# Kernel tuning notes

Hardware: AMD Instinct MI355X
Metric: run time of the kernel (lower is better)

Reference implementation:

```python
import jax, jax.numpy as jnp
import numpy as np

PAD = 0
B, C, N, W = 64, 4, 32, 32   # batch, max cross, max nodes/sample, max words/bag
D = 512                       # d_model == d_word_vec
DK = 64                       # attention dim
VOCAB = 32000


def setup_inputs() -> dict:
    key = jax.random.key(0)
    ks = jax.random.split(key, 10)
    token_ids = jax.random.randint(ks[0], (B, C, N, W), 1, VOCAB)
    node_lengths = jax.random.randint(ks[1], (B * C * N,), 1, W + 1)
    node_sizes = jax.random.randint(ks[2], (B * C,), 1, N + 1)
    cross_lengths = jax.random.randint(ks[3], (B,), 1, C + 1)
    con_hidden = jax.random.normal(ks[4], (B, D), dtype=jnp.float32)
    emb = jax.random.normal(ks[5], (VOCAB, D), dtype=jnp.float32) * 0.02
    emb = emb.at[PAD].set(0.0)  # padding_idx row is zero
    W_pre = jax.random.normal(ks[6], (D, DK), dtype=jnp.float32) / np.sqrt(D).astype(np.float32)
    b_pre = jnp.zeros((DK,), dtype=jnp.float32)
    W_q = jax.random.normal(ks[7], (D, DK), dtype=jnp.float32) / np.sqrt(D).astype(np.float32)
    v = jax.random.normal(ks[8], (DK,), dtype=jnp.float32) / np.sqrt(DK).astype(np.float32)
    return dict(token_ids=token_ids, node_lengths=node_lengths,
                node_sizes=node_sizes, cross_lengths=cross_lengths,
                con_hidden=con_hidden, emb=emb, W_pre=W_pre, b_pre=b_pre,
                W_q=W_q, v=v)


def reference(token_ids, node_lengths, node_sizes, cross_lengths,
              con_hidden, emb, W_pre, b_pre, W_q, v):
    # hidden: flattened context vector per cross/sample  [B, D]
    hidden = con_hidden.reshape(con_hidden.shape[0], -1)

    # --- fused ragged gather-and-pad (replaces nested python loops) ---
    # bags[t] = zero-padded stack of word embeddings for bag t; T = B*C*N
    bags = emb[token_ids.reshape(-1, W)]                         # [T, W, D]
    word_mask = jnp.arange(W)[None, :] < node_lengths[:, None]   # [T, W]
    bags = bags * word_mask[:, :, None].astype(bags.dtype)

    # root per bag = hidden[cross_idx] repeated for every bag of that sample
    roots = jnp.repeat(hidden, C * N, axis=0)                    # [T, D]

    # --- ConcatAttention(roots, bags) ---
    pre = jnp.einsum('twd,dk->twk', bags, W_pre) + b_pre         # [T, W, DK]
    q = roots @ W_q                                              # [T, DK]
    energy = jnp.einsum('twk,k->tw', jnp.tanh(pre + q[:, None, :]), v)
    score = jax.nn.softmax(energy, axis=1)                       # [T, W]
    context = jnp.einsum('tw,twd->td', score, bags)              # [T, D]

    # --- repack contexts into [B, max_cross, max_node_size, D], PAD(=0)-filled ---
    out = context.reshape(B, C, N, D)
    node_mask = jnp.arange(N)[None, :] < node_sizes.reshape(B, C)[:, :, None]  # [B,C,N]
    cross_mask = jnp.arange(C)[None, :] < cross_lengths[:, None]               # [B,C]
    mask = node_mask & cross_mask[:, :, None]
    out = out * mask[..., None].astype(out.dtype)
    return out, hidden
```

## Files before the change

### kernel.cpp

```cpp
#include <hip/hip_runtime.h>
#include <hip/hip_bf16.h>

#define TB   8192
#define WW   32
#define DD   512
#define DKK  64
#define CCC  4

#define CONV_BLKS   2000

using bf16x8 = __attribute__((ext_vector_type(8))) short;
using f32x4  = __attribute__((ext_vector_type(4))) float;
using f32x2  = __attribute__((ext_vector_type(2))) float;

__device__ __forceinline__ unsigned short f2bf(float x) {
    union { float f; unsigned u; } u;
    u.f = x;
    unsigned r = u.u + 0x7fffu + ((u.u >> 16) & 1u);
    return (unsigned short)(r >> 16);
}

__device__ __forceinline__ bf16x8 make_frag(float4 x, float4 y) {
    union { bf16x8 v; unsigned short s[8]; } u;
    u.s[0] = f2bf(x.x); u.s[1] = f2bf(x.y); u.s[2] = f2bf(x.z); u.s[3] = f2bf(x.w);
    u.s[4] = f2bf(y.x); u.s[5] = f2bf(y.y); u.s[6] = f2bf(y.z); u.s[7] = f2bf(y.w);
    return u.v;
}

__device__ __forceinline__ uint2 pack_fp8x8(float4 a, float4 b) {
    int lo = 0, hi = 0;
    lo = __builtin_amdgcn_cvt_pk_fp8_f32(a.x, a.y, lo, false);
    lo = __builtin_amdgcn_cvt_pk_fp8_f32(a.z, a.w, lo, true);
    hi = __builtin_amdgcn_cvt_pk_fp8_f32(b.x, b.y, hi, false);
    hi = __builtin_amdgcn_cvt_pk_fp8_f32(b.z, b.w, hi, true);
    uint2 r; r.x = (unsigned)lo; r.y = (unsigned)hi;
    return r;
}

__device__ __forceinline__ long long u2l(uint2 u) {
    union { uint2 v; long long l; } c; c.v = u; return c.l;
}

__device__ __forceinline__ void fp8x8_fma(float* cx, uint2 r, float s) {
    f32x2 f01 = __builtin_amdgcn_cvt_pk_f32_fp8((int)r.x, false);
    f32x2 f23 = __builtin_amdgcn_cvt_pk_f32_fp8((int)r.x, true);
    f32x2 f45 = __builtin_amdgcn_cvt_pk_f32_fp8((int)r.y, false);
    f32x2 f67 = __builtin_amdgcn_cvt_pk_f32_fp8((int)r.y, true);
    cx[0] += s * f01[0]; cx[1] += s * f01[1];
    cx[2] += s * f23[0]; cx[3] += s * f23[1];
    cx[4] += s * f45[0]; cx[5] += s * f45[1];
    cx[6] += s * f67[0]; cx[7] += s * f67[1];
}

__global__ __launch_bounds__(256) void preproc_kernel(
    const float* __restrict__ emb,
    unsigned char* __restrict__ emb8,
    const float* __restrict__ con_hidden,
    const float* __restrict__ W_q,
    float* __restrict__ qout,
    float* __restrict__ hid_out,
    const float* __restrict__ W_pre,
    uint2* __restrict__ wb8)
{
    const int blk = blockIdx.x;
    const int tid = threadIdx.x;
    if (blk < CONV_BLKS) {
        size_t idx = (size_t)blk * 256 + tid;
        #pragma unroll 4
        for (int it = 0; it < 4; ++it) {
            const size_t i = idx * 8;
            const float4* p = (const float4*)(emb + i);
            float4 a = p[0], b = p[1];
            *(uint2*)(emb8 + i) = pack_fp8x8(a, b);
            idx += (size_t)CONV_BLKS * 256;
        }
    } else if (blk < CONV_BLKS + 64) {
        if (tid >= 64) return;
        const int b = blk - CONV_BLKS;
        const int k = tid;
        const float* h = con_hidden + b * DD;
        float acc = 0.0f;
        #pragma unroll 8
        for (int d = 0; d < DD; ++d) acc += h[d] * W_q[d * DKK + k];
        qout[b * DKK + k] = acc;
        const float4* src = (const float4*)h;
        float4* dst = (float4*)(hid_out + b * DD);
        for (int i = k; i < DD / 4; i += 64) dst[i] = src[i];
    } else {
        if (tid >= 64) return;
        const int fb = blk - CONV_BLKS - 64;
        const int ks = fb >> 2, nt = fb & 3;
        const int lr = tid & 15, lg = tid >> 4;
        float w[8];
        #pragma unroll
        for (int j = 0; j < 8; ++j)
            w[j] = W_pre[(ks * 32 + lg * 8 + j) * DKK + nt * 16 + lr];
        wb8[fb * 64 + tid] = pack_fp8x8(float4{w[0], w[1], w[2], w[3]},
                                        float4{w[4], w[5], w[6], w[7]});
    }
}

__global__ __launch_bounds__(512) void bag_kernel(
    const int* __restrict__ token_ids,
    const int* __restrict__ node_lengths,
    const int* __restrict__ node_sizes,
    const int* __restrict__ cross_lengths,
    const unsigned char* __restrict__ emb8,
    const float* __restrict__ b_pre,
    const float* __restrict__ v,
    const float* __restrict__ q,
    const uint2* __restrict__ wb8,
    float* __restrict__ out)
{
    const int tid  = threadIdx.x;
    const int wid  = tid >> 6;
    const int lane = tid & 63;
    const int t = blockIdx.x * 8 + wid;
    const int b = t >> 7, cn = t & 127, c = cn >> 5, n = cn & 31;
    const int lr = lane & 15, lg = lane >> 4;

    __shared__ uint2 swb[4096];

    const int L = node_lengths[t];
    const int* toks = token_ids + t * WW;

    int my_tok = 0;
    if (lane < 32 && lane < L) my_tok = toks[lane];

    const int tok0 = __shfl(my_tok, lr);
    const int tok1 = __shfl(my_tok, 16 + lr);
    const unsigned char* hp0 = emb8 + ((size_t)tok0 << 9) + lg * 8;
    const unsigned char* hp1 = emb8 + ((size_t)tok1 << 9) + lg * 8;

    uint2 A0[8], A1[8], Bs[2][4];
    auto loadA = [&](int ks, int sl) {
        A0[sl] = *(const uint2*)(hp0 + ks * 32);
        A1[sl] = *(const uint2*)(hp1 + ks * 32);
    };
    auto loadB = [&](int ks, int sl) {
        #pragma unroll
        for (int nt = 0; nt < 4; ++nt)
            Bs[sl][nt] = swb[(ks * 4 + nt) * 64 + lane];
    };

    loadA(0, 0); loadA(1, 1); loadA(2, 2); loadA(3, 3);
    loadA(4, 4); loadA(5, 5); loadA(6, 6); loadA(7, 7);
    asm volatile("" ::: "memory");

    #pragma unroll
    for (int i = tid; i < 4096; i += 512) swb[i] = wb8[i];
    __syncthreads();

    f32x4 acc[2][4];
    #pragma unroll
    for (int mt = 0; mt < 2; ++mt)
        #pragma unroll
        for (int nt = 0; nt < 4; ++nt)
            acc[mt][nt] = (f32x4){0.f, 0.f, 0.f, 0.f};

    loadB(0, 0);
    asm volatile("" ::: "memory");

    #pragma unroll
    for (int ks = 0; ks < 16; ++ks) {
        long long a0 = u2l(A0[ks & 7]), a1 = u2l(A1[ks & 7]);
        if (ks + 8 < 16) loadA(ks + 8, ks & 7);
        if (ks + 1 < 16) loadB(ks + 1, (ks + 1) & 1);
        asm volatile("" ::: "memory");
        const int bs = ks & 1;
        long long b0 = u2l(Bs[bs][0]), b1 = u2l(Bs[bs][1]);
        long long b2 = u2l(Bs[bs][2]), b3 = u2l(Bs[bs][3]);
        acc[0][0] = __builtin_amdgcn_mfma_f32_16x16x32_fp8_fp8(a0, b0, acc[0][0], 0, 0, 0);
        acc[0][1] = __builtin_amdgcn_mfma_f32_16x16x32_fp8_fp8(a0, b1, acc[0][1], 0, 0, 0);
        acc[0][2] = __builtin_amdgcn_mfma_f32_16x16x32_fp8_fp8(a0, b2, acc[0][2], 0, 0, 0);
        acc[0][3] = __builtin_amdgcn_mfma_f32_16x16x32_fp8_fp8(a0, b3, acc[0][3], 0, 0, 0);
        acc[1][0] = __builtin_amdgcn_mfma_f32_16x16x32_fp8_fp8(a1, b0, acc[1][0], 0, 0, 0);
        acc[1][1] = __builtin_amdgcn_mfma_f32_16x16x32_fp8_fp8(a1, b1, acc[1][1], 0, 0, 0);
        acc[1][2] = __builtin_amdgcn_mfma_f32_16x16x32_fp8_fp8(a1, b2, acc[1][2], 0, 0, 0);
        acc[1][3] = __builtin_amdgcn_mfma_f32_16x16x32_fp8_fp8(a1, b3, acc[1][3], 0, 0, 0);
    }

    const int d0 = lane * 8;
    uint2 R[6];
    auto cissue = [&](int w, int sl) {
        int tk = __shfl(my_tok, w);
        R[sl] = *(const uint2*)(emb8 + ((size_t)tk << 9) + d0);
    };
    cissue(0, 0); cissue(1, 1); cissue(2, 2);
    cissue(3, 3); cissue(4, 4); cissue(5, 5);
    asm volatile("" ::: "memory");

    float qb[4], vv[4];
    #pragma unroll
    for (int nt = 0; nt < 4; ++nt) {
        int cidx = nt * 16 + lr;
        qb[nt] = q[b * DKK + cidx] + b_pre[cidx];
        vv[nt] = v[cidx];
    }
    float ev[8];
    #pragma unroll
    for (int mt = 0; mt < 2; ++mt) {
        #pragma unroll
        for (int r = 0; r < 4; ++r) {
            float s = 0.0f;
            #pragma unroll
            for (int nt = 0; nt < 4; ++nt) {
                float pre = acc[mt][nt][r] + qb[nt];
                float ez = __expf(2.0f * pre);
                float th = 1.0f - 2.0f * __builtin_amdgcn_rcpf(ez + 1.0f);
                s += th * vv[nt];
            }
            s += __shfl_xor(s, 1);
            s += __shfl_xor(s, 2);
            s += __shfl_xor(s, 4);
            s += __shfl_xor(s, 8);
            ev[mt * 4 + r] = s;
        }
    }

    float mx = ev[0];
    #pragma unroll
    for (int j = 1; j < 8; ++j) mx = fmaxf(mx, ev[j]);
    mx = fmaxf(mx, __shfl_xor(mx, 16));
    mx = fmaxf(mx, __shfl_xor(mx, 32));
    float sc[8], sm = 0.0f;
    #pragma unroll
    for (int j = 0; j < 8; ++j) { sc[j] = __expf(ev[j] - mx); sm += sc[j]; }
    sm += __shfl_xor(sm, 16);
    sm += __shfl_xor(sm, 32);
    const float inv = 1.0f / sm;
    #pragma unroll
    for (int j = 0; j < 8; ++j) sc[j] *= inv;

    float cx[8];
    #pragma unroll
    for (int j = 0; j < 8; ++j) cx[j] = 0.0f;

    #pragma unroll
    for (int w = 0; w < WW; ++w) {
        uint2 r = R[w % 6];
        float s = __shfl(sc[(w >> 4) * 4 + (w & 3)], ((w >> 2) & 3) * 16);
        if (w + 6 < WW) cissue(w + 6, (w + 6) % 6);
        asm volatile("" ::: "memory");
        fp8x8_fma(cx, r, s);
    }

    const bool outmask = (n < node_sizes[b * CCC + c]) && (c < cross_lengths[b]);
    if (!outmask) {
        #pragma unroll
        for (int j = 0; j < 8; ++j) cx[j] = 0.0f;
    }
    float4* op = (float4*)(out + (size_t)t * DD + d0);
    op[0] = float4{cx[0], cx[1], cx[2], cx[3]};
    op[1] = float4{cx[4], cx[5], cx[6], cx[7]};
}

__global__ __launch_bounds__(64) void prep_kernel(
    const float* __restrict__ con_hidden, const float* __restrict__ W_q,
    float* __restrict__ qout, float* __restrict__ hid_out)
{
    const int b = blockIdx.x;
    const int k = threadIdx.x;
    const float* h = con_hidden + b * DD;
    float acc = 0.0f;
    #pragma unroll 8
    for (int d = 0; d < DD; ++d) acc += h[d] * W_q[d * DKK + k];
    qout[b * DKK + k] = acc;
    const float4* src = (const float4*)h;
    float4* dst = (float4*)(hid_out + b * DD);
    for (int i = k; i < DD / 4; i += 64) dst[i] = src[i];
}

__global__ __launch_bounds__(64) void pack_wpre(
    const float* __restrict__ W_pre, bf16x8* __restrict__ wb)
{
    const int blk = blockIdx.x;
    const int ks = blk >> 2, nt = blk & 3;
    const int l  = threadIdx.x;
    const int lr = l & 15, lg = l >> 4;
    union { bf16x8 v; unsigned short s[8]; } u;
    #pragma unroll
    for (int j = 0; j < 8; ++j) {
        int k = ks * 32 + lg * 8 + j;
        u.s[j] = f2bf(W_pre[k * DKK + nt * 16 + lr]);
    }
    wb[blk * 64 + l] = u.v;
}

__global__ __launch_bounds__(256) void bag_kernel_f32(
    const int* __restrict__ token_ids, const int* __restrict__ node_lengths,
    const int* __restrict__ node_sizes, const int* __restrict__ cross_lengths,
    const float* __restrict__ embf, const float* __restrict__ b_pre,
    const float* __restrict__ v, const float* __restrict__ q,
    const bf16x8* __restrict__ wb, float* __restrict__ out)
{
    const int wid  = threadIdx.x >> 6;
    const int lane = threadIdx.x & 63;
    const int t = blockIdx.x * 4 + wid;
    const int b = t >> 7, cn = t & 127, c = cn >> 5, n = cn & 31;
    const int lr = lane & 15, lg = lane >> 4;

    const int L = node_lengths[t];
    const int* toks = token_ids + t * WW;
    int my_tok = 0;
    if (lane < 32 && lane < L) my_tok = toks[lane];
    const int tok0 = __shfl(my_tok, lr);
    const int tok1 = __shfl(my_tok, 16 + lr);
    const float* fp0 = embf + ((size_t)tok0 << 9) + lg * 8;
    const float* fp1 = embf + ((size_t)tok1 << 9) + lg * 8;

    f32x4 acc[2][4];
    #pragma unroll
    for (int mt = 0; mt < 2; ++mt)
        #pragma unroll
        for (int nt = 0; nt < 4; ++nt)
            acc[mt][nt] = (f32x4){0.f, 0.f, 0.f, 0.f};

    #pragma unroll 4
    for (int ks = 0; ks < 16; ++ks) {
        const float4* a0p = (const float4*)(fp0 + ks * 32);
        const float4* a1p = (const float4*)(fp1 + ks * 32);
        bf16x8 a0 = make_frag(a0p[0], a0p[1]);
        bf16x8 a1 = make_frag(a1p[0], a1p[1]);
        #pragma unroll
        for (int nt = 0; nt < 4; ++nt) {
            bf16x8 bb = wb[(ks * 4 + nt) * 64 + lane];
            acc[0][nt] = __builtin_amdgcn_mfma_f32_16x16x32_bf16(a0, bb, acc[0][nt], 0, 0, 0);
            acc[1][nt] = __builtin_amdgcn_mfma_f32_16x16x32_bf16(a1, bb, acc[1][nt], 0, 0, 0);
        }
    }

    float qb[4], vv[4];
    #pragma unroll
    for (int nt = 0; nt < 4; ++nt) {
        int cidx = nt * 16 + lr;
        qb[nt] = q[b * DKK + cidx] + b_pre[cidx];
        vv[nt] = v[cidx];
    }
    float ev[8];
    #pragma unroll
    for (int mt = 0; mt < 2; ++mt) {
        #pragma unroll
        for (int r = 0; r < 4; ++r) {
            float s = 0.0f;
            #pragma unroll
            for (int nt = 0; nt < 4; ++nt) {
                float pre = acc[mt][nt][r] + qb[nt];
                float ez = __expf(2.0f * pre);
                float th = 1.0f - 2.0f * __builtin_amdgcn_rcpf(ez + 1.0f);
                s += th * vv[nt];
            }
            s += __shfl_xor(s, 1); s += __shfl_xor(s, 2);
            s += __shfl_xor(s, 4); s += __shfl_xor(s, 8);
            ev[mt * 4 + r] = s;
        }
    }
    float mx = ev[0];
    #pragma unroll
    for (int j = 1; j < 8; ++j) mx = fmaxf(mx, ev[j]);
    mx = fmaxf(mx, __shfl_xor(mx, 16));
    mx = fmaxf(mx, __shfl_xor(mx, 32));
    float sc[8], sm = 0.0f;
    #pragma unroll
    for (int j = 0; j < 8; ++j) { sc[j] = __expf(ev[j] - mx); sm += sc[j]; }
    sm += __shfl_xor(sm, 16); sm += __shfl_xor(sm, 32);
    const float inv = 1.0f / sm;
    #pragma unroll
    for (int j = 0; j < 8; ++j) sc[j] *= inv;

    const int d0 = lane * 8;
    float cx[8];
    #pragma unroll
    for (int j = 0; j < 8; ++j) cx[j] = 0.0f;
    #pragma unroll
    for (int w = 0; w < WW; ++w) {
        int tk = __shfl(my_tok, w);
        float s = __shfl(sc[(w >> 4) * 4 + (w & 3)], ((w >> 2) & 3) * 16);
        const float4* pr = (const float4*)(embf + ((size_t)tk << 9) + d0);
        float4 x0 = pr[0], x1 = pr[1];
        cx[0] += s * x0.x; cx[1] += s * x0.y; cx[2] += s * x0.z; cx[3] += s * x0.w;
        cx[4] += s * x1.x; cx[5] += s * x1.y; cx[6] += s * x1.z; cx[7] += s * x1.w;
    }
    const bool outmask = (n < node_sizes[b * CCC + c]) && (c < cross_lengths[b]);
    if (!outmask) {
        #pragma unroll
        for (int j = 0; j < 8; ++j) cx[j] = 0.0f;
    }
    float4* op = (float4*)(out + (size_t)t * DD + d0);
    op[0] = float4{cx[0], cx[1], cx[2], cx[3]};
    op[1] = float4{cx[4], cx[5], cx[6], cx[7]};
}

extern "C" void kernel_launch(void* const* d_in, const int* in_sizes, int n_in,
                              void* d_out, int out_size, void* d_ws, size_t ws_size,
                              hipStream_t stream) {
    const int*   token_ids     = (const int*)d_in[0];
    const int*   node_lengths  = (const int*)d_in[1];
    const int*   node_sizes    = (const int*)d_in[2];
    const int*   cross_lengths = (const int*)d_in[3];
    const float* con_hidden    = (const float*)d_in[4];
    const float* emb           = (const float*)d_in[5];
    const float* W_pre         = (const float*)d_in[6];
    const float* b_pre         = (const float*)d_in[7];
    const float* W_q           = (const float*)d_in[8];
    const float* v             = (const float*)d_in[9];

    float*  out     = (float*)d_out;
    float*  hid_out = out + (size_t)TB * DD;
    float*  q       = (float*)d_ws;
    uint2*  wb8     = (uint2*)((char*)d_ws + 16 * 1024);
    bf16x8* wb      = (bf16x8*)((char*)d_ws + 16 * 1024);
    unsigned char* emb8 = (unsigned char*)d_ws + 80 * 1024;

    const size_t need = 80 * 1024 + (size_t)32000 * DD;

    if (ws_size >= need) {
        preproc_kernel<<<CONV_BLKS + 128, 256, 0, stream>>>(
            emb, emb8, con_hidden, W_q, q, hid_out, W_pre, wb8);
        bag_kernel<<<TB / 8, 512, 0, stream>>>(
            token_ids, node_lengths, node_sizes, cross_lengths,
            emb8, b_pre, v, q, wb8, out);
    } else {
        prep_kernel<<<64, 64, 0, stream>>>(con_hidden, W_q, q, hid_out);
        pack_wpre<<<64, 64, 0, stream>>>(W_pre, wb);
        bag_kernel_f32<<<TB / 4, 256, 0, stream>>>(
            token_ids, node_lengths, node_sizes, cross_lengths,
            emb, b_pre, v, q, wb, out);
    }
}
```

Measured before the change: 74.26 us.

## Precompute per-vocab W_pre projection table instead of per-token MFMA GEMM in bags

Because pre = emb[tok] @ W_pre depends only on the token, the change computes a 32000x64 projection table P once (fused with the fp8 conversion of the embedding table) and has the bag kernel gather P rows instead of running per-bag MFMA GEMMs. This removes 8192x32 redundant 512x64 products and the shared-memory weight staging in the bag kernel. The trade-off is an extra 8 MB write and an extra kernel launch over the full vocabulary, and the energy reduction now uses a full 64-lane shuffle per word. The q projection prep is also split across 4 thread quarters with a shared reduction.

```diff
diff --git a/kernel.cpp b/kernel.cpp
--- a/kernel.cpp
+++ b/kernel.cpp
@@ -6,8 +6,7 @@
 #define DD   512
 #define DKK  64
 #define CCC  4
-
-#define CONV_BLKS   2000
+#define VCB  32000
 
 using bf16x8 = __attribute__((ext_vector_type(8))) short;
 using f32x4  = __attribute__((ext_vector_type(4))) float;
@@ -52,43 +51,36 @@
     cx[6] += s * f67[0]; cx[7] += s * f67[1];
 }
 
-__global__ __launch_bounds__(256) void preproc_kernel(
-    const float* __restrict__ emb,
-    unsigned char* __restrict__ emb8,
+__global__ __launch_bounds__(256) void prep_pack(
     const float* __restrict__ con_hidden,
     const float* __restrict__ W_q,
+    const float* __restrict__ W_pre,
     float* __restrict__ qout,
     float* __restrict__ hid_out,
-    const float* __restrict__ W_pre,
     uint2* __restrict__ wb8)
 {
     const int blk = blockIdx.x;
     const int tid = threadIdx.x;
-    if (blk < CONV_BLKS) {
-        size_t idx = (size_t)blk * 256 + tid;
-        #pragma unroll 4
-        for (int it = 0; it < 4; ++it) {
-            const size_t i = idx * 8;
-            const float4* p = (const float4*)(emb + i);
-            float4 a = p[0], b = p[1];
-            *(uint2*)(emb8 + i) = pack_fp8x8(a, b);
-            idx += (size_t)CONV_BLKS * 256;
-        }
-    } else if (blk < CONV_BLKS + 64) {
-        if (tid >= 64) return;
-        const int b = blk - CONV_BLKS;
-        const int k = tid;
+    if (blk < 64) {
+        __shared__ float red[256];
+        const int b = blk;
+        const int k = tid & 63, qtr = tid >> 6;
         const float* h = con_hidden + b * DD;
         float acc = 0.0f;
+        const int d0 = qtr * 128;
         #pragma unroll 8
-        for (int d = 0; d < DD; ++d) acc += h[d] * W_q[d * DKK + k];
-        qout[b * DKK + k] = acc;
-        const float4* src = (const float4*)h;
-        float4* dst = (float4*)(hid_out + b * DD);
-        for (int i = k; i < DD / 4; i += 64) dst[i] = src[i];
+        for (int d = 0; d < 128; ++d) acc += h[d0 + d] * W_q[(d0 + d) * DKK + k];
+        red[tid] = acc;
+        __syncthreads();
+        if (tid < 64)
+            qout[b * DKK + tid] = red[tid] + red[64 + tid] + red[128 + tid] + red[192 + tid];
+        if (tid < 128) {
+            const float4* src = (const float4*)h;
+            ((float4*)(hid_out + b * DD))[tid] = src[tid];
+        }
     } else {
         if (tid >= 64) return;
-        const int fb = blk - CONV_BLKS - 64;
+        const int fb = blk - 64;
         const int ks = fb >> 2, nt = fb & 3;
         const int lr = tid & 15, lg = tid >> 4;
         float w[8];
@@ -98,6 +90,51 @@
         wb8[fb * 64 + tid] = pack_fp8x8(float4{w[0], w[1], w[2], w[3]},
                                         float4{w[4], w[5], w[6], w[7]});
     }
+}
+
+__global__ __launch_bounds__(256) void conv_gemm(
+    const float* __restrict__ emb,
+    unsigned char* __restrict__ emb8,
+    float* __restrict__ P,
+    const uint2* __restrict__ wb8)
+{
+    const int tid  = threadIdx.x;
+    const int wid  = tid >> 6;
+    const int lane = tid & 63;
+    const int lr = lane & 15, lg = lane >> 4;
+    const int base = blockIdx.x * 64 + wid * 16;
+
+    __shared__ uint2 swb[4096];
+    #pragma unroll
+    for (int i = tid; i < 4096; i += 256) swb[i] = wb8[i];
+    __syncthreads();
+
+    const float* arow = emb + (size_t)(base + lr) * DD + lg * 8;
+    unsigned char* erow = emb8 + (size_t)(base + lr) * DD + lg * 8;
+
+    f32x4 accP[4];
+    #pragma unroll
+    for (int nt = 0; nt < 4; ++nt) accP[nt] = (f32x4){0.f, 0.f, 0.f, 0.f};
+
+    #pragma unroll 4
+    for (int ks = 0; ks < 16; ++ks) {
+        const float4* p = (const float4*)(arow + ks * 32);
+        float4 x = p[0], y = p[1];
+        uint2 a8 = pack_fp8x8(x, y);
+        *(uint2*)(erow + ks * 32) = a8;
+        long long a = u2l(a8);
+        #pragma unroll
+        for (int nt = 0; nt < 4; ++nt) {
+            long long bfr = u2l(swb[(ks * 4 + nt) * 64 + lane]);
+            accP[nt] = __builtin_amdgcn_mfma_f32_16x16x32_fp8_fp8(a, bfr, accP[nt], 0, 0, 0);
+        }
+    }
+
+    #pragma unroll
+    for (int nt = 0; nt < 4; ++nt)
+        #pragma unroll
+        for (int r = 0; r < 4; ++r)
+            P[(size_t)(base + lg * 4 + r) * DKK + nt * 16 + lr] = accP[nt][r];
 }
 
 __global__ __launch_bounds__(512) void bag_kernel(
@@ -106,10 +143,10 @@
     const int* __restrict__ node_sizes,
     const int* __restrict__ cross_lengths,
     const unsigned char* __restrict__ emb8,
+    const float* __restrict__ P,
     const float* __restrict__ b_pre,
     const float* __restrict__ v,
     const float* __restrict__ q,
-    const uint2* __restrict__ wb8,
     float* __restrict__ out)
 {
     const int tid  = threadIdx.x;
@@ -117,9 +154,6 @@
     const int lane = tid & 63;
     const int t = blockIdx.x * 8 + wid;
     const int b = t >> 7, cn = t & 127, c = cn >> 5, n = cn & 31;
-    const int lr = lane & 15, lg = lane >> 4;
-
-    __shared__ uint2 swb[4096];
 
     const int L = node_lengths[t];
     const int* toks = token_ids + t * WW;
@@ -127,58 +161,17 @@
     int my_tok = 0;
     if (lane < 32 && lane < L) my_tok = toks[lane];
 
-    const int tok0 = __shfl(my_tok, lr);
-    const int tok1 = __shfl(my_tok, 16 + lr);
-    const unsigned char* hp0 = emb8 + ((size_t)tok0 << 9) + lg * 8;
-    const unsigned char* hp1 = emb8 + ((size_t)tok1 << 9) + lg * 8;
-
-    uint2 A0[8], A1[8], Bs[2][4];
-    auto loadA = [&](int ks, int sl) {
-        A0[sl] = *(const uint2*)(hp0 + ks * 32);
-        A1[sl] = *(const uint2*)(hp1 + ks * 32);
+    const float qb = q[b * DKK + lane] + b_pre[lane];
+    const float vv = v[lane];
+
+    float Pv[8];
+    auto pissue = [&](int w, int sl) {
+        int tk = __shfl(my_tok, w);
+        Pv[sl] = P[(size_t)tk * DKK + lane];
     };
-    auto loadB = [&](int ks, int sl) {
-        #pragma unroll
-        for (int nt = 0; nt < 4; ++nt)
-            Bs[sl][nt] = swb[(ks * 4 + nt) * 64 + lane];
-    };
-
-    loadA(0, 0); loadA(1, 1); loadA(2, 2); loadA(3, 3);
-    loadA(4, 4); loadA(5, 5); loadA(6, 6); loadA(7, 7);
+    pissue(0, 0); pissue(1, 1); pissue(2, 2); pissue(3, 3);
+    pissue(4, 4); pissue(5, 5); pissue(6, 6); pissue(7, 7);
     asm volatile("" ::: "memory");
-
-    #pragma unroll
-    for (int i = tid; i < 4096; i += 512) swb[i] = wb8[i];
-    __syncthreads();
-
-    f32x4 acc[2][4];
-    #pragma unroll
-    for (int mt = 0; mt < 2; ++mt)
-        #pragma unroll
-        for (int nt = 0; nt < 4; ++nt)
-            acc[mt][nt] = (f32x4){0.f, 0.f, 0.f, 0.f};
-
-    loadB(0, 0);
-    asm volatile("" ::: "memory");
-
-    #pragma unroll
-    for (int ks = 0; ks < 16; ++ks) {
-        long long a0 = u2l(A0[ks & 7]), a1 = u2l(A1[ks & 7]);
-        if (ks + 8 < 16) loadA(ks + 8, ks & 7);
-        if (ks + 1 < 16) loadB(ks + 1, (ks + 1) & 1);
-        asm volatile("" ::: "memory");
-        const int bs = ks & 1;
-        long long b0 = u2l(Bs[bs][0]), b1 = u2l(Bs[bs][1]);
-        long long b2 = u2l(Bs[bs][2]), b3 = u2l(Bs[bs][3]);
-        acc[0][0] = __builtin_amdgcn_mfma_f32_16x16x32_fp8_fp8(a0, b0, acc[0][0], 0, 0, 0);
-        acc[0][1] = __builtin_amdgcn_mfma_f32_16x16x32_fp8_fp8(a0, b1, acc[0][1], 0, 0, 0);
-        acc[0][2] = __builtin_amdgcn_mfma_f32_16x16x32_fp8_fp8(a0, b2, acc[0][2], 0, 0, 0);
-        acc[0][3] = __builtin_amdgcn_mfma_f32_16x16x32_fp8_fp8(a0, b3, acc[0][3], 0, 0, 0);
-        acc[1][0] = __builtin_amdgcn_mfma_f32_16x16x32_fp8_fp8(a1, b0, acc[1][0], 0, 0, 0);
-        acc[1][1] = __builtin_amdgcn_mfma_f32_16x16x32_fp8_fp8(a1, b1, acc[1][1], 0, 0, 0);
-        acc[1][2] = __builtin_amdgcn_mfma_f32_16x16x32_fp8_fp8(a1, b2, acc[1][2], 0, 0, 0);
-        acc[1][3] = __builtin_amdgcn_mfma_f32_16x16x32_fp8_fp8(a1, b3, acc[1][3], 0, 0, 0);
-    }
 
     const int d0 = lane * 8;
     uint2 R[6];
@@ -190,47 +183,30 @@
     cissue(3, 3); cissue(4, 4); cissue(5, 5);
     asm volatile("" ::: "memory");
 
-    float qb[4], vv[4];
-    #pragma unroll
-    for (int nt = 0; nt < 4; ++nt) {
-        int cidx = nt * 16 + lr;
-        qb[nt] = q[b * DKK + cidx] + b_pre[cidx];
-        vv[nt] = v[cidx];
-    }
-    float ev[8];
-    #pragma unroll
-    for (int mt = 0; mt < 2; ++mt) {
-        #pragma unroll
-        for (int r = 0; r < 4; ++r) {
-            float s = 0.0f;
-            #pragma unroll
-            for (int nt = 0; nt < 4; ++nt) {
-                float pre = acc[mt][nt][r] + qb[nt];
-                float ez = __expf(2.0f * pre);
-                float th = 1.0f - 2.0f * __builtin_amdgcn_rcpf(ez + 1.0f);
-                s += th * vv[nt];
-            }
-            s += __shfl_xor(s, 1);
-            s += __shfl_xor(s, 2);
-            s += __shfl_xor(s, 4);
-            s += __shfl_xor(s, 8);
-            ev[mt * 4 + r] = s;
-        }
-    }
-
-    float mx = ev[0];
-    #pragma unroll
-    for (int j = 1; j < 8; ++j) mx = fmaxf(mx, ev[j]);
-    mx = fmaxf(mx, __shfl_xor(mx, 16));
-    mx = fmaxf(mx, __shfl_xor(mx, 32));
-    float sc[8], sm = 0.0f;
-    #pragma unroll
-    for (int j = 0; j < 8; ++j) { sc[j] = __expf(ev[j] - mx); sm += sc[j]; }
-    sm += __shfl_xor(sm, 16);
-    sm += __shfl_xor(sm, 32);
+    float sc[32];
+    #pragma unroll
+    for (int w = 0; w < WW; ++w) {
+        float pv = Pv[w & 7];
+        if (w + 8 < WW) pissue(w + 8, w & 7);
+        asm volatile("" ::: "memory");
+        float ez = __expf(2.0f * (pv + qb));
+        float th = 1.0f - 2.0f * __builtin_amdgcn_rcpf(ez + 1.0f);
+        float e = th * vv;
+        e += __shfl_xor(e, 1);  e += __shfl_xor(e, 2);
+        e += __shfl_xor(e, 4);  e += __shfl_xor(e, 8);
+        e += __shfl_xor(e, 16); e += __shfl_xor(e, 32);
+        sc[w] = e;
+    }
+
+    float mx = sc[0];
+    #pragma unroll
+    for (int j = 1; j < 32; ++j) mx = fmaxf(mx, sc[j]);
+    float sm = 0.0f;
+    #pragma unroll
+    for (int j = 0; j < 32; ++j) { sc[j] = __expf(sc[j] - mx); sm += sc[j]; }
     const float inv = 1.0f / sm;
     #pragma unroll
-    for (int j = 0; j < 8; ++j) sc[j] *= inv;
+    for (int j = 0; j < 32; ++j) sc[j] *= inv;
 
     float cx[8];
     #pragma unroll
@@ -239,7 +215,7 @@
     #pragma unroll
     for (int w = 0; w < WW; ++w) {
         uint2 r = R[w % 6];
-        float s = __shfl(sc[(w >> 4) * 4 + (w & 3)], ((w >> 2) & 3) * 16);
+        float s = sc[w];
         if (w + 6 < WW) cissue(w + 6, (w + 6) % 6);
         asm volatile("" ::: "memory");
         fp8x8_fma(cx, r, s);
@@ -410,16 +386,17 @@
     float*  q       = (float*)d_ws;
     uint2*  wb8     = (uint2*)((char*)d_ws + 16 * 1024);
     bf16x8* wb      = (bf16x8*)((char*)d_ws + 16 * 1024);
-    unsigned char* emb8 = (unsigned char*)d_ws + 80 * 1024;
-
-    const size_t need = 80 * 1024 + (size_t)32000 * DD;
+    float*  P       = (float*)((char*)d_ws + 80 * 1024);
+    unsigned char* emb8 = (unsigned char*)d_ws + 80 * 1024 + (size_t)VCB * DKK * 4;
+
+    const size_t need = 80 * 1024 + (size_t)VCB * DKK * 4 + (size_t)VCB * DD;
 
     if (ws_size >= need) {
-        preproc_kernel<<<CONV_BLKS + 128, 256, 0, stream>>>(
-            emb, emb8, con_hidden, W_q, q, hid_out, W_pre, wb8);
+        prep_pack<<<128, 256, 0, stream>>>(con_hidden, W_q, W_pre, q, hid_out, wb8);
+        conv_gemm<<<VCB / 64, 256, 0, stream>>>(emb, emb8, P, wb8);
         bag_kernel<<<TB / 8, 512, 0, stream>>>(
             token_ids, node_lengths, node_sizes, cross_lengths,
-            emb8, b_pre, v, q, wb8, out);
+            emb8, P, b_pre, v, q, out);
     } else {
         prep_kernel<<<64, 64, 0, stream>>>(con_hidden, W_q, q, hid_out);
         pack_wpre<<<64, 64, 0, stream>>>(W_pre, wb);
```

Result: faster. 67.37 us (-9.3%).
